# Kernel optimization log

Measured on AMD Instinct MI355X. Metric: run time of the kernel, lower is better.

## Reference

```python
import jax, jax.numpy as jnp
import numpy as np

T_STEP = 0.01
N_STEPS = 1000
H_S = 64
N_TARGETS = 2048
INPUT_S = 2
H_NN = 256
ACTION_S = 2


def setup_inputs() -> dict:
    key = jax.random.key(0)
    ks = jax.random.split(key, 9)
    target = jax.random.normal(ks[0], (N_TARGETS, INPUT_S), dtype=jnp.float32)
    D = jax.random.normal(ks[1], (H_S,), dtype=jnp.float32) * 0.1
    P = jax.random.normal(ks[2], (H_S, H_S), dtype=jnp.float32)
    l1_w = jax.random.normal(ks[3], (H_NN, INPUT_S), dtype=jnp.float32) * 0.05
    l1_b = jax.random.normal(ks[4], (H_NN,), dtype=jnp.float32) * 0.05
    l2_w = jax.random.normal(ks[5], (H_S, H_NN), dtype=jnp.float32) * 0.05
    l2_b = jax.random.normal(ks[6], (H_S,), dtype=jnp.float32) * 0.05
    lm_w = jax.random.normal(ks[7], (ACTION_S, H_S), dtype=jnp.float32) * 0.05
    lm_b = jax.random.normal(ks[8], (ACTION_S,), dtype=jnp.float32) * 0.05
    return {"target": target, "D": D, "P": P,
            "l1_w": l1_w, "l1_b": l1_b, "l2_w": l2_w, "l2_b": l2_b,
            "lm_w": lm_w, "lm_b": lm_b}


def reference(target, D, P, l1_w, l1_b, l2_w, l2_b, lm_w, lm_b):
    # initial condition MLP: relu(l1) -> l2, then transpose to (h_s, n_targets)
    h = jax.nn.relu(target @ l1_w.T + l1_b)           # (n_targets, h_nn)
    x0 = (h @ l2_w.T + l2_b).T                        # (h_s, n_targets)
    # A = P diag(exp(D)) P^-1 ; step map x <- (I - dt*A) x
    A = (P * jnp.exp(D)[None, :]) @ jnp.linalg.inv(P)  # (h_s, h_s)
    M = jnp.eye(H_S, dtype=A.dtype) - T_STEP * A

    def step(x, _):
        act = jnp.tanh(x.T @ lm_w.T + lm_b)            # (n_targets, action_s)
        return M @ x, (x, act)

    _, (hidden_states, acts) = jax.lax.scan(step, x0, None, length=N_STEPS)
    # hidden_states: (n_steps, h_s, n_targets); acts: (n_steps, n_targets, action_s)
    actions = jnp.transpose(acts, (1, 2, 0))           # (n_targets, action_s, n_steps)
    return actions, hidden_states
```

## Files before the change

### kernel.cpp

```cpp
#include <hip/hip_runtime.h>
#include <math.h>

#define NT 2048
#define HS 64
#define HNN 256
#define NSTEPS 1000
#define TSTEP 0.01f

typedef unsigned short u16;
typedef __attribute__((ext_vector_type(8))) short bf16x8;
typedef __attribute__((ext_vector_type(4))) float f32x4;

#define OFF_HT   148736

#define S_H 1028

__device__ inline void bsplit(float x, u16& hi, u16& lo) {
    unsigned u = __float_as_uint(x);
    unsigned r = (u + 0x7FFFu + ((u >> 16) & 1u)) >> 16;
    hi = (u16)r;
    float xh = __uint_as_float(r << 16);
    float d = x - xh;
    unsigned v = __float_as_uint(d);
    unsigned s = (v + 0x7FFFu + ((v >> 16) & 1u)) >> 16;
    lo = (u16)s;
}

__device__ inline void bar_lds() {
    asm volatile("s_waitcnt lgkmcnt(0)" ::: "memory");
    __builtin_amdgcn_s_barrier();
    asm volatile("" ::: "memory");
}

__device__ inline float tanh_fast(float x) {
    float xc = fminf(fmaxf(x, -15.f), 15.f);
    float a = __builtin_amdgcn_exp2f(xc * 2.885390082f);
    return (a - 1.f) * __builtin_amdgcn_rcpf(a + 1.f);
}

struct FrontSh {
    union {
        float Aug[64 * 130];
        struct {
            union { float shT[256 * 17]; float rs[64 * 17]; float us[8 * 128]; } a;
            float x0s[64 * 17];
            float y0s[64 * 17];
        } p2;
    } u;
    float Rs[64 * 65];
    float fvec[2][64];
    float tgt[8][2];
    float lam_s[64], l2l_s[64];
    float Q_s[128];
};

__global__ __launch_bounds__(512) void k_front(const float* __restrict__ target,
                                               const float* __restrict__ l1_w,
                                               const float* __restrict__ l1_b,
                                               const float* __restrict__ l2_w,
                                               const float* __restrict__ l2_b,
                                               const float* __restrict__ lm_w,
                                               const float* __restrict__ lm_b,
                                               const float* __restrict__ D,
                                               const float* __restrict__ P,
                                               float* __restrict__ ws,
                                               float* __restrict__ actions) {
    __shared__ FrontSh sh;
    int ct = blockIdx.x;
    int cbase = ct * 8;
    int tid = threadIdx.x;
    float* Aug = sh.u.Aug;

    for (int idx = tid; idx < 64 * 128; idx += 512) {
        int r = idx >> 7, c = idx & 127;
        Aug[r * 130 + c] = (c < 64) ? P[r * 64 + c] : ((c - 64) == r ? 1.f : 0.f);
    }
    __syncthreads();

    if (tid < 64) {
        float nv = Aug[tid * 130];
        float pv = __shfl(nv, 0);
        sh.fvec[0][tid] = (tid == 0) ? 0.f : nv * __builtin_amdgcn_rcpf(pv);
    } else if (tid < 128) {
        int i = tid - 64;
        float l = 1.0f - TSTEP * expf(D[i]);
        sh.lam_s[i] = l;
        sh.l2l_s[i] = log2f(l);
    } else if (tid < 256) {
        int t = tid - 128;
        int a = t >> 6, i = t & 63;
        float s = 0.f;
        for (int r = 0; r < 64; ++r) s = fmaf(lm_w[a * 64 + r], P[r * 64 + i], s);
        sh.Q_s[t] = s;
    } else if (tid < 264) {
        int c = tid - 256;
        float2 tv = ((const float2*)target)[cbase + c];
        sh.tgt[c][0] = tv.x; sh.tgt[c][1] = tv.y;
    }
    __syncthreads();

    for (int t = 0; t < 64; ++t) {
        int par = t & 1;
        if (tid < 64) {
            int col0 = (t < 63) ? (t + 1) : 64;
            float f = sh.fvec[par][tid];
            float src = Aug[t * 130 + col0];
            float nv = Aug[tid * 130 + col0] - f * src;
            Aug[tid * 130 + col0] = nv;
            if (t < 63) {
                float pv = __shfl(nv, t + 1);
                sh.fvec[par ^ 1][tid] = (tid == (t + 1)) ? 0.f
                                        : nv * __builtin_amdgcn_rcpf(pv);
            }
        } else {
            int w = (tid >> 6) - 1;
            int lane = tid & 63;
            float f = sh.fvec[par][lane];
            const float* rowp = Aug + t * 130;
            float* rowr = Aug + lane * 130;
            int pcnt = 63 - t;
            for (int s = 1 + w; s < 64; s += 7) {
                int col = (s < pcnt) ? (t + 1 + s) : (64 + (s - pcnt));
                rowr[col] -= f * rowp[col];
            }
        }
        __syncthreads();
    }

    for (int idx = tid; idx < 4096; idx += 512) {
        int j = idx >> 6, m = idx & 63;
        sh.Rs[j * 65 + m] = Aug[j * 130 + 64 + m]
                            * __builtin_amdgcn_rcpf(Aug[j * 130 + j]);
    }
    __syncthreads();

    if (tid < 256) {
        float w0 = l1_w[2 * tid], w1 = l1_w[2 * tid + 1], bb = l1_b[tid];
        #pragma unroll
        for (int cc = 0; cc < 8; ++cc)
            sh.u.p2.a.shT[tid * 17 + cc] =
                fmaxf(fmaf(w0, sh.tgt[cc][0], fmaf(w1, sh.tgt[cc][1], bb)), 0.f);
    }
    __syncthreads();

    int i = tid >> 3, c = tid & 7;
    {
        const float* l2wi = l2_w + i * 256;
        float a0 = l2_b[i], a1 = 0, a2 = 0, a3 = 0;
        #pragma unroll 4
        for (int j = 0; j < 256; j += 4) {
            a0 = fmaf(l2wi[j],     sh.u.p2.a.shT[j * 17 + c],       a0);
            a1 = fmaf(l2wi[j + 1], sh.u.p2.a.shT[(j + 1) * 17 + c], a1);
            a2 = fmaf(l2wi[j + 2], sh.u.p2.a.shT[(j + 2) * 17 + c], a2);
            a3 = fmaf(l2wi[j + 3], sh.u.p2.a.shT[(j + 3) * 17 + c], a3);
        }
        sh.u.p2.x0s[i * 17 + c] = (a0 + a1) + (a2 + a3);
    }
    __syncthreads();

    const float* Ri = sh.Rs + i * 65;
    {
        float b0 = 0, b1 = 0;
        #pragma unroll 4
        for (int m = 0; m < 64; m += 2) {
            b0 = fmaf(Ri[m],     sh.u.p2.x0s[m * 17 + c],       b0);
            b1 = fmaf(Ri[m + 1], sh.u.p2.x0s[(m + 1) * 17 + c], b1);
        }
        sh.u.p2.y0s[i * 17 + c] = b0 + b1;
    }
    __syncthreads();

    const float* Pi = P + i * 64;
    #pragma unroll 1
    for (int it = 0; it < 2; ++it) {
        float r0 = sh.u.p2.x0s[i * 17 + c], r1 = 0;
        #pragma unroll 4
        for (int m = 0; m < 64; m += 2) {
            r0 = fmaf(-Pi[m],     sh.u.p2.y0s[m * 17 + c],       r0);
            r1 = fmaf(-Pi[m + 1], sh.u.p2.y0s[(m + 1) * 17 + c], r1);
        }
        __syncthreads();
        sh.u.p2.a.rs[i * 17 + c] = r0 + r1;
        __syncthreads();
        float d0 = 0, d1 = 0;
        #pragma unroll 4
        for (int m = 0; m < 64; m += 2) {
            d0 = fmaf(Ri[m],     sh.u.p2.a.rs[m * 17 + c],       d0);
            d1 = fmaf(Ri[m + 1], sh.u.p2.a.rs[(m + 1) * 17 + c], d1);
        }
        sh.u.p2.y0s[i * 17 + c] += d0 + d1;
        __syncthreads();
    }

    for (int idx = tid; idx < 1024; idx += 512) {
        int cgi = idx >> 7, t = idx & 127;
        sh.u.p2.a.us[cgi * 128 + t] = sh.Q_s[t] * sh.u.p2.y0s[(t & 63) * 17 + cgi];
    }
    if (tid < 128) {
        int kt = tid >> 6, lane = tid & 63;
        int c15 = lane & 15;
        if ((c15 >> 3) == (ct & 1)) {
            int cl = c15 & 7;
            int i0 = kt * 32 + (lane >> 4) * 8;
            u16* YH = (u16*)(ws + OFF_HT);
            u16* YL = YH + 131072;
            bf16x8 vh, vl;
            #pragma unroll
            for (int j = 0; j < 8; ++j) {
                u16 h, lo;
                bsplit(sh.u.p2.y0s[(i0 + j) * 17 + cl], h, lo);
                vh[j] = (short)h; vl[j] = (short)lo;
            }
            int off = (((ct >> 1) * 2 + kt) * 64 + lane);
            *(bf16x8*)(YH + off * 8) = vh;
            *(bf16x8*)(YL + off * 8) = vl;
        }
    }
    __syncthreads();

    if (tid < 500) {
        int k0 = tid * 2;
        float b0 = lm_b[0], b1 = lm_b[1];
        float fk0 = (float)k0;
        float2 s[8][2];
        #pragma unroll
        for (int j = 0; j < 8; ++j) {
            s[j][0] = make_float2(b0, b0);
            s[j][1] = make_float2(b1, b1);
        }
        #pragma unroll 2
        for (int ii = 0; ii < 64; ++ii) {
            float p0 = __builtin_amdgcn_exp2f(fk0 * sh.l2l_s[ii]);
            float p1 = p0 * sh.lam_s[ii];
            #pragma unroll
            for (int j = 0; j < 8; ++j) {
                float u0 = sh.u.p2.a.us[j * 128 + ii];
                float u1 = sh.u.p2.a.us[j * 128 + 64 + ii];
                s[j][0].x = fmaf(u0, p0, s[j][0].x);
                s[j][0].y = fmaf(u0, p1, s[j][0].y);
                s[j][1].x = fmaf(u1, p0, s[j][1].x);
                s[j][1].y = fmaf(u1, p1, s[j][1].y);
            }
        }
        #pragma unroll
        for (int j = 0; j < 8; ++j)
            #pragma unroll
            for (int a = 0; a < 2; ++a) {
                float2 r;
                r.x = tanh_fast(s[j][a].x);
                r.y = tanh_fast(s[j][a].y);
                *(float2*)(actions + (size_t)(cbase + j) * 2000 + a * 1000 + k0) = r;
            }
    }
}

__global__ __launch_bounds__(512, 2) void k_hidden(const float* __restrict__ P,
                                                   const float* __restrict__ D,
                                                   const float* __restrict__ ws,
                                                   float* __restrict__ hidden) {
    int k = blockIdx.x;
    int tid = threadIdx.x;
    int wid = tid >> 6, lane = tid & 63;
    int l15 = lane & 15, lg = lane >> 4;

    extern __shared__ float stage[];
    __shared__ float lp_s[64];

    const u16* YH = (const u16*)(ws + OFF_HT);
    const u16* YL = YH + 131072;

    if (tid < 64) {
        float l = 1.0f - TSTEP * expf(D[tid]);
        lp_s[tid] = exp2f((float)k * log2f(l));
    }
    __syncthreads();

    bf16x8 ah[4][2], al[4][2];
    #pragma unroll
    for (int rt = 0; rt < 4; ++rt) {
        int r = rt * 16 + l15;
        #pragma unroll
        for (int kt = 0; kt < 2; ++kt) {
            int i0 = kt * 32 + lg * 8;
            #pragma unroll
            for (int j = 0; j < 8; ++j) {
                float v = P[r * 64 + i0 + j] * lp_s[i0 + j];
                u16 h, lo;
                bsplit(v, h, lo);
                ah[rt][kt][j] = (short)h;
                al[rt][kt][j] = (short)lo;
            }
        }
    }

    float* outk = hidden + (size_t)k * 64 * NT;

    #pragma unroll 1
    for (int half = 0; half < 2; ++half) {
        bf16x8 bh[8][2], bl[8][2];
        #pragma unroll
        for (int q = 0; q < 8; ++q)
            #pragma unroll
            for (int kt = 0; kt < 2; ++kt) {
                int ct_g = half * 64 + wid * 8 + q;
                int off = ((ct_g * 2 + kt) * 64 + lane) * 8;
                bh[q][kt] = *(const bf16x8*)(YH + off);
                bl[q][kt] = *(const bf16x8*)(YL + off);
            }
        #pragma unroll
        for (int rt = 0; rt < 4; ++rt) {
            #pragma unroll
            for (int q = 0; q < 8; ++q) {
                f32x4 acc = {0.f, 0.f, 0.f, 0.f};
                #pragma unroll
                for (int kt = 0; kt < 2; ++kt) {
                    acc = __builtin_amdgcn_mfma_f32_16x16x32_bf16(ah[rt][kt], bh[q][kt], acc, 0, 0, 0);
                    acc = __builtin_amdgcn_mfma_f32_16x16x32_bf16(al[rt][kt], bh[q][kt], acc, 0, 0, 0);
                    acc = __builtin_amdgcn_mfma_f32_16x16x32_bf16(ah[rt][kt], bl[q][kt], acc, 0, 0, 0);
                }
                int col = wid * 128 + q * 16 + l15;
                #pragma unroll
                for (int reg = 0; reg < 4; ++reg)
                    stage[(lg * 4 + reg) * S_H + col] = acc[reg];
            }
            bar_lds();
            #pragma unroll
            for (int it = 0; it < 8; ++it) {
                int f = it * 512 + tid;
                int r = f >> 8, c4 = f & 255;
                float4 v = *(const float4*)&stage[r * S_H + (c4 << 2)];
                *(float4*)(outk + (size_t)(rt * 16 + r) * NT + half * 1024 + (c4 << 2)) = v;
            }
            bar_lds();
        }
    }
}

extern "C" void kernel_launch(void* const* d_in, const int* in_sizes, int n_in,
                              void* d_out, int out_size, void* d_ws, size_t ws_size,
                              hipStream_t stream) {
    const float* target = (const float*)d_in[0];
    const float* D      = (const float*)d_in[1];
    const float* P      = (const float*)d_in[2];
    const float* l1_w   = (const float*)d_in[3];
    const float* l1_b   = (const float*)d_in[4];
    const float* l2_w   = (const float*)d_in[5];
    const float* l2_b   = (const float*)d_in[6];
    const float* lm_w   = (const float*)d_in[7];
    const float* lm_b   = (const float*)d_in[8];
    float* ws = (float*)d_ws;
    float* actions = (float*)d_out;
    float* hidden  = (float*)d_out + 4096000;

    hipFuncSetAttribute((const void*)k_hidden,
                        hipFuncAttributeMaxDynamicSharedMemorySize, 16 * S_H * 4);

    hipLaunchKernelGGL(k_front,  dim3(256),  dim3(512), 0, stream,
                       target, l1_w, l1_b, l2_w, l2_b, lm_w, lm_b, D, P, ws, actions);
    hipLaunchKernelGGL(k_hidden, dim3(1000), dim3(512), 16 * S_H * 4, stream, P, D, ws, hidden);
}
```

Baseline: 185.2 us.

## Solve P y = x0 directly by Gaussian elimination instead of inverting P

Replaces the full 64x64 matrix inversion (augmented with identity, 128 columns) plus R*x0 products and two iterative-refinement passes with a direct Gaussian elimination on P augmented by the 8 x0 columns of the block. This removes the identity half of the elimination work and the later matvec and refinement stages with their barriers. The shared memory layout shrinks accordingly. The cost is the loss of the refinement steps, which may reduce accuracy of y0 for an ill-conditioned P.

After: 165.5 us, median of 2. 10.6% less time.

```diff
diff --git a/kernel.cpp b/kernel.cpp
--- a/kernel.cpp
+++ b/kernel.cpp
@@ -39,19 +39,14 @@
 }
 
 struct FrontSh {
-    union {
-        float Aug[64 * 130];
-        struct {
-            union { float shT[256 * 17]; float rs[64 * 17]; float us[8 * 128]; } a;
-            float x0s[64 * 17];
-            float y0s[64 * 17];
-        } p2;
-    } u;
-    float Rs[64 * 65];
+    float Aug[64 * 73];
+    float shT[256 * 9];
+    float y0s[64 * 9];
     float fvec[2][64];
     float tgt[8][2];
     float lam_s[64], l2l_s[64];
     float Q_s[128];
+    float us[8 * 128];
 };
 
 __global__ __launch_bounds__(512) void k_front(const float* __restrict__ target,
@@ -69,68 +64,26 @@
     int ct = blockIdx.x;
     int cbase = ct * 8;
     int tid = threadIdx.x;
-    float* Aug = sh.u.Aug;
-
-    for (int idx = tid; idx < 64 * 128; idx += 512) {
-        int r = idx >> 7, c = idx & 127;
-        Aug[r * 130 + c] = (c < 64) ? P[r * 64 + c] : ((c - 64) == r ? 1.f : 0.f);
-    }
-    __syncthreads();
-
-    if (tid < 64) {
-        float nv = Aug[tid * 130];
-        float pv = __shfl(nv, 0);
-        sh.fvec[0][tid] = (tid == 0) ? 0.f : nv * __builtin_amdgcn_rcpf(pv);
-    } else if (tid < 128) {
-        int i = tid - 64;
+
+    for (int idx = tid; idx < 4096; idx += 512) {
+        int r = idx >> 6, c = idx & 63;
+        sh.Aug[r * 73 + c] = P[r * 64 + c];
+    }
+    if (tid >= 448 && tid < 456) {
+        int c = tid - 448;
+        float2 tv = ((const float2*)target)[cbase + c];
+        sh.tgt[c][0] = tv.x; sh.tgt[c][1] = tv.y;
+    } else if (tid >= 256 && tid < 320) {
+        int i = tid - 256;
         float l = 1.0f - TSTEP * expf(D[i]);
         sh.lam_s[i] = l;
         sh.l2l_s[i] = log2f(l);
-    } else if (tid < 256) {
-        int t = tid - 128;
+    } else if (tid >= 320 && tid < 448) {
+        int t = tid - 320;
         int a = t >> 6, i = t & 63;
         float s = 0.f;
         for (int r = 0; r < 64; ++r) s = fmaf(lm_w[a * 64 + r], P[r * 64 + i], s);
         sh.Q_s[t] = s;
-    } else if (tid < 264) {
-        int c = tid - 256;
-        float2 tv = ((const float2*)target)[cbase + c];
-        sh.tgt[c][0] = tv.x; sh.tgt[c][1] = tv.y;
-    }
-    __syncthreads();
-
-    for (int t = 0; t < 64; ++t) {
-        int par = t & 1;
-        if (tid < 64) {
-            int col0 = (t < 63) ? (t + 1) : 64;
-            float f = sh.fvec[par][tid];
-            float src = Aug[t * 130 + col0];
-            float nv = Aug[tid * 130 + col0] - f * src;
-            Aug[tid * 130 + col0] = nv;
-            if (t < 63) {
-                float pv = __shfl(nv, t + 1);
-                sh.fvec[par ^ 1][tid] = (tid == (t + 1)) ? 0.f
-                                        : nv * __builtin_amdgcn_rcpf(pv);
-            }
-        } else {
-            int w = (tid >> 6) - 1;
-            int lane = tid & 63;
-            float f = sh.fvec[par][lane];
-            const float* rowp = Aug + t * 130;
-            float* rowr = Aug + lane * 130;
-            int pcnt = 63 - t;
-            for (int s = 1 + w; s < 64; s += 7) {
-                int col = (s < pcnt) ? (t + 1 + s) : (64 + (s - pcnt));
-                rowr[col] -= f * rowp[col];
-            }
-        }
-        __syncthreads();
-    }
-
-    for (int idx = tid; idx < 4096; idx += 512) {
-        int j = idx >> 6, m = idx & 63;
-        sh.Rs[j * 65 + m] = Aug[j * 130 + 64 + m]
-                            * __builtin_amdgcn_rcpf(Aug[j * 130 + j]);
     }
     __syncthreads();
 
@@ -138,7 +91,7 @@
         float w0 = l1_w[2 * tid], w1 = l1_w[2 * tid + 1], bb = l1_b[tid];
         #pragma unroll
         for (int cc = 0; cc < 8; ++cc)
-            sh.u.p2.a.shT[tid * 17 + cc] =
+            sh.shT[tid * 9 + cc] =
                 fmaxf(fmaf(w0, sh.tgt[cc][0], fmaf(w1, sh.tgt[cc][1], bb)), 0.f);
     }
     __syncthreads();
@@ -149,52 +102,56 @@
         float a0 = l2_b[i], a1 = 0, a2 = 0, a3 = 0;
         #pragma unroll 4
         for (int j = 0; j < 256; j += 4) {
-            a0 = fmaf(l2wi[j],     sh.u.p2.a.shT[j * 17 + c],       a0);
-            a1 = fmaf(l2wi[j + 1], sh.u.p2.a.shT[(j + 1) * 17 + c], a1);
-            a2 = fmaf(l2wi[j + 2], sh.u.p2.a.shT[(j + 2) * 17 + c], a2);
-            a3 = fmaf(l2wi[j + 3], sh.u.p2.a.shT[(j + 3) * 17 + c], a3);
-        }
-        sh.u.p2.x0s[i * 17 + c] = (a0 + a1) + (a2 + a3);
-    }
-    __syncthreads();
-
-    const float* Ri = sh.Rs + i * 65;
-    {
-        float b0 = 0, b1 = 0;
-        #pragma unroll 4
-        for (int m = 0; m < 64; m += 2) {
-            b0 = fmaf(Ri[m],     sh.u.p2.x0s[m * 17 + c],       b0);
-            b1 = fmaf(Ri[m + 1], sh.u.p2.x0s[(m + 1) * 17 + c], b1);
-        }
-        sh.u.p2.y0s[i * 17 + c] = b0 + b1;
-    }
-    __syncthreads();
-
-    const float* Pi = P + i * 64;
-    #pragma unroll 1
-    for (int it = 0; it < 2; ++it) {
-        float r0 = sh.u.p2.x0s[i * 17 + c], r1 = 0;
-        #pragma unroll 4
-        for (int m = 0; m < 64; m += 2) {
-            r0 = fmaf(-Pi[m],     sh.u.p2.y0s[m * 17 + c],       r0);
-            r1 = fmaf(-Pi[m + 1], sh.u.p2.y0s[(m + 1) * 17 + c], r1);
+            a0 = fmaf(l2wi[j],     sh.shT[j * 9 + c],       a0);
+            a1 = fmaf(l2wi[j + 1], sh.shT[(j + 1) * 9 + c], a1);
+            a2 = fmaf(l2wi[j + 2], sh.shT[(j + 2) * 9 + c], a2);
+            a3 = fmaf(l2wi[j + 3], sh.shT[(j + 3) * 9 + c], a3);
+        }
+        sh.Aug[i * 73 + 64 + c] = (a0 + a1) + (a2 + a3);
+    }
+    if (tid < 64) {
+        float nv = sh.Aug[tid * 73];
+        float pv = __shfl(nv, 0);
+        sh.fvec[0][tid] = (tid == 0) ? 0.f : nv * __builtin_amdgcn_rcpf(pv);
+    }
+    __syncthreads();
+
+    for (int t = 0; t < 64; ++t) {
+        int par = t & 1;
+        if (tid < 64) {
+            int col0 = (t < 63) ? (t + 1) : 64;
+            float f = sh.fvec[par][tid];
+            float src = sh.Aug[t * 73 + col0];
+            float nv = sh.Aug[tid * 73 + col0] - f * src;
+            sh.Aug[tid * 73 + col0] = nv;
+            if (t < 63) {
+                float pv = __shfl(nv, t + 1);
+                sh.fvec[par ^ 1][tid] = (tid == (t + 1)) ? 0.f
+                                        : nv * __builtin_amdgcn_rcpf(pv);
+            }
+        } else {
+            int w = (tid >> 6) - 1;
+            int lane = tid & 63;
+            float f = sh.fvec[par][lane];
+            const float* rowp = sh.Aug + t * 73;
+            float* rowr = sh.Aug + lane * 73;
+            int pcnt = 62 - t;
+            int smax = pcnt + 8;
+            for (int s = 1 + w; s <= smax; s += 7) {
+                int col = (s <= pcnt) ? (t + 1 + s) : (64 + (s - pcnt - 1));
+                rowr[col] -= f * rowp[col];
+            }
         }
         __syncthreads();
-        sh.u.p2.a.rs[i * 17 + c] = r0 + r1;
-        __syncthreads();
-        float d0 = 0, d1 = 0;
-        #pragma unroll 4
-        for (int m = 0; m < 64; m += 2) {
-            d0 = fmaf(Ri[m],     sh.u.p2.a.rs[m * 17 + c],       d0);
-            d1 = fmaf(Ri[m + 1], sh.u.p2.a.rs[(m + 1) * 17 + c], d1);
-        }
-        sh.u.p2.y0s[i * 17 + c] += d0 + d1;
-        __syncthreads();
-    }
+    }
+
+    sh.y0s[i * 9 + c] = sh.Aug[i * 73 + 64 + c]
+                        * __builtin_amdgcn_rcpf(sh.Aug[i * 73 + i]);
+    __syncthreads();
 
     for (int idx = tid; idx < 1024; idx += 512) {
         int cgi = idx >> 7, t = idx & 127;
-        sh.u.p2.a.us[cgi * 128 + t] = sh.Q_s[t] * sh.u.p2.y0s[(t & 63) * 17 + cgi];
+        sh.us[cgi * 128 + t] = sh.Q_s[t] * sh.y0s[(t & 63) * 9 + cgi];
     }
     if (tid < 128) {
         int kt = tid >> 6, lane = tid & 63;
@@ -208,7 +165,7 @@
             #pragma unroll
             for (int j = 0; j < 8; ++j) {
                 u16 h, lo;
-                bsplit(sh.u.p2.y0s[(i0 + j) * 17 + cl], h, lo);
+                bsplit(sh.y0s[(i0 + j) * 9 + cl], h, lo);
                 vh[j] = (short)h; vl[j] = (short)lo;
             }
             int off = (((ct >> 1) * 2 + kt) * 64 + lane);
@@ -234,8 +191,8 @@
             float p1 = p0 * sh.lam_s[ii];
             #pragma unroll
             for (int j = 0; j < 8; ++j) {
-                float u0 = sh.u.p2.a.us[j * 128 + ii];
-                float u1 = sh.u.p2.a.us[j * 128 + 64 + ii];
+                float u0 = sh.us[j * 128 + ii];
+                float u1 = sh.us[j * 128 + 64 + ii];
                 s[j][0].x = fmaf(u0, p0, s[j][0].x);
                 s[j][0].y = fmaf(u0, p1, s[j][0].y);
                 s[j][1].x = fmaf(u1, p0, s[j][1].x);
```
